# Performance work log

Measured on AMD Instinct MI355X. Metric: run time of the kernel, lower is better.

## Reference

```python
import jax, jax.numpy as jnp
import numpy as np

NEG_INF = -9e15  # matches the -9000000000000000.0 mask constant in the torch code
ALPHA = 0.2      # LeakyReLU negative slope


def setup_inputs() -> dict:
    key = jax.random.key(0)
    ks = jax.random.split(key, 8)
    N, F = 8192, 256
    h = jax.random.normal(ks[0], (N, F), dtype=jnp.float32)
    adj = jax.random.randint(ks[1], (N, N), 0, 2).astype(jnp.float32)
    W = jax.random.normal(ks[2], (F, F), dtype=jnp.float32) * 0.05
    a = jax.random.normal(ks[3], (2 * F, 1), dtype=jnp.float32) * 0.05
    w_ih = jax.random.normal(ks[4], (3 * F, F), dtype=jnp.float32) * 0.05
    w_hh = jax.random.normal(ks[5], (3 * F, F), dtype=jnp.float32) * 0.05
    b_ih = jax.random.normal(ks[6], (3 * F,), dtype=jnp.float32) * 0.05
    b_hh = jax.random.normal(ks[7], (3 * F,), dtype=jnp.float32) * 0.05
    return {"h": h, "adj": adj, "W": W, "a": a,
            "w_ih": w_ih, "w_hh": w_hh, "b_ih": b_ih, "b_hh": b_hh}


def reference(h, adj, W, a, w_ih, w_hh, b_ih, b_hh):
    F_out = W.shape[1]
    Wh = h @ W  # [N, F]
    # a_input @ a decomposes exactly: e_ij = leakyrelu(Wh_i . a[:F] + Wh_j . a[F:])
    src = Wh @ a[:F_out]   # [N, 1]
    dst = Wh @ a[F_out:]   # [N, 1]
    e = jax.nn.leaky_relu(src + dst.T, ALPHA)          # [N, N]
    att = jnp.where(adj > 0, e, NEG_INF)
    att = jax.nn.softmax(att, axis=1)                   # dropout: eval mode (identity)
    h_prime = att @ Wh                                  # [N, F]
    # torch GRUCell(h_prime, h)
    gi = h_prime @ w_ih.T + b_ih                        # [N, 3F]
    gh = h @ w_hh.T + b_hh
    i_r, i_z, i_n = jnp.split(gi, 3, axis=1)
    h_r, h_z, h_n = jnp.split(gh, 3, axis=1)
    r = jax.nn.sigmoid(i_r + h_r)
    z = jax.nn.sigmoid(i_z + h_z)
    n = jnp.tanh(i_n + r * h_n)
    return (1.0 - z) * n + z * h
```

## Files before the change

kernel.cpp:

```cpp
#include <hip/hip_runtime.h>

typedef __attribute__((ext_vector_type(8))) short bf16x8;
typedef __attribute__((ext_vector_type(4))) float f32x4;
typedef unsigned short u16;

#define NN 8192
#define FD 256

__device__ __forceinline__ u16 f2bf(float f) {
  union { float f; unsigned u; } v; v.f = f;
  unsigned r = v.u + 0x7FFF + ((v.u >> 16) & 1);
  return (u16)(r >> 16);
}

__device__ __forceinline__ bf16x8 ldcvt8(const float* __restrict__ p) {
  f32x4 x0 = *(const f32x4*)p;
  f32x4 x1 = *(const f32x4*)(p + 4);
  bf16x8 t;
  t[0] = (short)f2bf(x0[0]); t[1] = (short)f2bf(x0[1]);
  t[2] = (short)f2bf(x0[2]); t[3] = (short)f2bf(x0[3]);
  t[4] = (short)f2bf(x1[0]); t[5] = (short)f2bf(x1[1]);
  t[6] = (short)f2bf(x1[2]); t[7] = (short)f2bf(x1[3]);
  return t;
}

__global__ __launch_bounds__(256) void k_zero(float* __restrict__ p) {
  size_t g = (size_t)(blockIdx.x * 256 + threadIdx.x) * 4;
  f32x4 z = {0.f, 0.f, 0.f, 0.f};
  *(f32x4*)(p + g) = z;
}

__global__ __launch_bounds__(256) void k_wh(const float* __restrict__ h,
                                            const float* __restrict__ W,
                                            const float* __restrict__ a,
                                            u16* __restrict__ whT,
                                            float* __restrict__ src,
                                            float* __restrict__ dst) {
  int tid = threadIdx.x;
  int lane = tid & 63;
  int wv = tid >> 6;
  int r0 = blockIdx.x * 64 + (wv >> 1) * 32;
  int c0 = blockIdx.y * 64 + (wv & 1) * 32;
  int lr = lane & 15;
  int q = lane >> 4;

  f32x4 acc[2][2] = {};
  for (int kk = 0; kk < FD; kk += 32) {
    int kb = kk + q * 8;
    bf16x8 av[2], bv[2];
#pragma unroll
    for (int m = 0; m < 2; m++)
      av[m] = ldcvt8(h + (size_t)(r0 + m * 16 + lr) * FD + kb);
#pragma unroll
    for (int n = 0; n < 2; n++) {
      int col = c0 + n * 16 + lr;
      const float* p = W + (size_t)kb * FD + col;
      bf16x8 t;
#pragma unroll
      for (int e = 0; e < 8; e++) t[e] = (short)f2bf(p[(size_t)e * FD]);
      bv[n] = t;
    }
#pragma unroll
    for (int m = 0; m < 2; m++)
#pragma unroll
      for (int n = 0; n < 2; n++)
        acc[m][n] = __builtin_amdgcn_mfma_f32_16x16x32_bf16(av[m], bv[n], acc[m][n], 0, 0, 0);
  }
#pragma unroll
  for (int m = 0; m < 2; m++)
#pragma unroll
    for (int n = 0; n < 2; n++) {
      int gc = c0 + n * 16 + lr;
      int gr = r0 + m * 16 + q * 4;
      ushort4 st;
      st.x = f2bf(acc[m][n][0]);
      st.y = f2bf(acc[m][n][1]);
      st.z = f2bf(acc[m][n][2]);
      st.w = f2bf(acc[m][n][3]);
      *(ushort4*)(whT + (size_t)gc * NN + gr) = st;
    }
  float aA0 = a[c0 + lr], aA1 = a[c0 + 16 + lr];
  float aB0 = a[256 + c0 + lr], aB1 = a[256 + c0 + 16 + lr];
#pragma unroll
  for (int m = 0; m < 2; m++)
#pragma unroll
    for (int j = 0; j < 4; j++) {
      float s1 = acc[m][0][j] * aA0 + acc[m][1][j] * aA1;
      float s2 = acc[m][0][j] * aB0 + acc[m][1][j] * aB1;
#pragma unroll
      for (int sh = 1; sh < 16; sh <<= 1) {
        s1 += __shfl_xor(s1, sh);
        s2 += __shfl_xor(s2, sh);
      }
      if (lr == 0) {
        int row = r0 + m * 16 + q * 4 + j;
        atomicAdd(&src[row], s1);
        atomicAdd(&dst[row], s2);
      }
    }
}

__global__ __launch_bounds__(512, 4) void k_att(const float* __restrict__ adj,
                                                const u16* __restrict__ whT,
                                                const float* __restrict__ src,
                                                const float* __restrict__ dst,
                                                float* __restrict__ hp,
                                                float* __restrict__ lg) {
  __shared__ u16 pbuf[3][4096];
  __shared__ float dst_lds[2048];
  __shared__ float lred[8][64];

  const int tid = threadIdx.x;
  const int lane = tid & 63;
  const int w = tid >> 6;
  const int lr = lane & 15;
  const int q = lane >> 4;
  const int bid = blockIdx.x;
  const int jh = bid & 3;
  const int i0 = (bid >> 2) * 64;
  const int jb = jh * 2048;

  const int pi = lane;
  const float* adjP = adj + (size_t)(i0 + pi) * NN + jb + w * 8;
  const float srcv = src[i0 + pi];
  const int c0 = w * 32;
  const u16* wp = whT + (size_t)(c0 + lr) * NN + jb + q * 8;
  const int pw = (pi * 64 + w * 8) ^ ((pi & 7) << 3);

  f32x4 ar0[2], ar1[2];
  bf16x8 B0[2][2], B1[2][2];
  f32x4 acc[4][2] = {};
  float lsum = 0.f;

  *(f32x4*)&dst_lds[tid * 4] = *(const f32x4*)(dst + jb + tid * 4);

#define AL(S, AR)                                                              \
  { AR[0] = *(const f32x4*)(adjP + (size_t)(S) * 64);                          \
    AR[1] = *(const f32x4*)(adjP + (size_t)(S) * 64 + 4); }
#define BL(S, B)                                                               \
  { _Pragma("unroll") for (int kh = 0; kh < 2; kh++)                           \
    _Pragma("unroll") for (int n = 0; n < 2; n++)                              \
      B[kh][n] = *(const bf16x8*)(wp + (size_t)n * 16 * NN + (S) * 64 + kh * 32); }
#define PS(S, AR, WB)                                                          \
  {                                                                            \
    bf16x8 s0;                                                                 \
    _Pragma("unroll") for (int v = 0; v < 2; v++)                              \
      _Pragma("unroll") for (int e = 0; e < 4; e++) {                          \
        float x = srcv + dst_lds[(S) * 64 + w * 8 + v * 4 + e];                \
        x = fmaxf(x, 0.2f * x);                                                \
        float p = AR[v][e] * __expf(x);                                        \
        lsum += p;                                                             \
        s0[v * 4 + e] = (short)f2bf(p);                                        \
      }                                                                        \
    *(bf16x8*)&pbuf[WB][pw] = s0;                                              \
  }
#define CMPS(RB, B)                                                            \
  {                                                                            \
    _Pragma("unroll") for (int m = 0; m < 4; m++)                              \
      _Pragma("unroll") for (int kh = 0; kh < 2; kh++) {                       \
        bf16x8 pf = *(const bf16x8*)&pbuf[RB][((m * 16 + lr) * 64 + kh * 32 + q * 8) ^ ((lr & 7) << 3)]; \
        acc[m][0] = __builtin_amdgcn_mfma_f32_16x16x32_bf16(pf, B[kh][0], acc[m][0], 0, 0, 0); \
        acc[m][1] = __builtin_amdgcn_mfma_f32_16x16x32_bf16(pf, B[kh][1], acc[m][1], 0, 0, 0); \
      }                                                                        \
  }
#define LBAR asm volatile("s_waitcnt lgkmcnt(0)\n\ts_barrier" ::: "memory")

  AL(0, ar0);
  AL(1, ar1);
  BL(0, B0);
  __syncthreads();
  PS(0, ar0, 0);
  LBAR;

  int rb = 0, wb = 1;
  for (int t = 0; t < 32; t += 2) {
    if (t + 2 < 32) AL(t + 2, ar0);
    PS(t + 1, ar1, wb);
    BL(t + 1, B1);
    CMPS(rb, B0);
    LBAR;
    rb = wb; wb = (wb == 2) ? 0 : wb + 1;
    if (t + 3 < 32) AL(t + 3, ar1);
    if (t + 2 < 32) {
      PS(t + 2, ar0, wb);
      BL(t + 2, B0);
    }
    CMPS(rb, B1);
    LBAR;
    rb = wb; wb = (wb == 2) ? 0 : wb + 1;
  }
#undef AL
#undef BL
#undef PS
#undef CMPS
#undef LBAR

  lred[w][pi] = lsum;
  __syncthreads();
  if (tid < 64) {
    float l = 0.f;
#pragma unroll
    for (int v = 0; v < 8; v++) l += lred[v][tid];
    atomicAdd(&lg[i0 + tid], l);
  }
#pragma unroll
  for (int m = 0; m < 4; m++)
#pragma unroll
    for (int n = 0; n < 2; n++)
#pragma unroll
      for (int j = 0; j < 4; j++)
        atomicAdd(&hp[(size_t)(i0 + m * 16 + q * 4 + j) * FD + c0 + n * 16 + lr],
                  acc[m][n][j]);
}

__global__ __launch_bounds__(256) void k_norm(const float* __restrict__ hp,
                                              const float* __restrict__ lg,
                                              u16* __restrict__ hpb) {
  int g = blockIdx.x * 1024 + threadIdx.x * 4;
  f32x4 v = *(const f32x4*)(hp + g);
  float inv = 1.0f / lg[g >> 8];
  ushort4 st;
  st.x = f2bf(v[0] * inv);
  st.y = f2bf(v[1] * inv);
  st.z = f2bf(v[2] * inv);
  st.w = f2bf(v[3] * inv);
  *(ushort4*)(hpb + g) = st;
}

__global__ __launch_bounds__(256) void k_gru(const u16* __restrict__ hpb,
                                             const float* __restrict__ h,
                                             const float* __restrict__ wih,
                                             const float* __restrict__ whh,
                                             const float* __restrict__ bih,
                                             const float* __restrict__ bhh,
                                             float* __restrict__ out) {
  int tid = threadIdx.x;
  int lane = tid & 63;
  int wv = tid >> 6;
  int i0 = blockIdx.x * 32;
  int lr = lane & 15;
  int q = lane >> 4;
  int c = blockIdx.y * 64 + wv * 16 + lr;
  f32x4 gi[3][2] = {};
  f32x4 gh[3][2] = {};
  for (int kk = 0; kk < FD; kk += 32) {
    int kb = kk + q * 8;
    bf16x8 ap[2], ah[2], bi[3], bh[3];
#pragma unroll
    for (int m = 0; m < 2; m++) {
      ap[m] = *(const bf16x8*)(hpb + (size_t)(i0 + m * 16 + lr) * FD + kb);
      ah[m] = ldcvt8(h + (size_t)(i0 + m * 16 + lr) * FD + kb);
    }
#pragma unroll
    for (int g = 0; g < 3; g++) {
      bi[g] = ldcvt8(wih + (size_t)(g * 256 + c) * FD + kb);
      bh[g] = ldcvt8(whh + (size_t)(g * 256 + c) * FD + kb);
    }
#pragma unroll
    for (int g = 0; g < 3; g++)
#pragma unroll
      for (int m = 0; m < 2; m++) {
        gi[g][m] = __builtin_amdgcn_mfma_f32_16x16x32_bf16(ap[m], bi[g], gi[g][m], 0, 0, 0);
        gh[g][m] = __builtin_amdgcn_mfma_f32_16x16x32_bf16(ah[m], bh[g], gh[g][m], 0, 0, 0);
      }
  }
  float bir = bih[c], biz = bih[256 + c], bin = bih[512 + c];
  float bhr = bhh[c], bhz = bhh[256 + c], bhn = bhh[512 + c];
#pragma unroll
  for (int m = 0; m < 2; m++)
#pragma unroll
    for (int j = 0; j < 4; j++) {
      int row = i0 + m * 16 + q * 4 + j;
      float rv = gi[0][m][j] + bir + gh[0][m][j] + bhr;
      float zv = gi[1][m][j] + biz + gh[1][m][j] + bhz;
      float r = 1.f / (1.f + __expf(-rv));
      float z = 1.f / (1.f + __expf(-zv));
      float nx = gi[2][m][j] + bin + r * (gh[2][m][j] + bhn);
      float n = 1.f - 2.f / (__expf(2.f * nx) + 1.f);
      float hv = h[(size_t)row * FD + c];
      out[(size_t)row * FD + c] = (1.f - z) * n + z * hv;
    }
}

extern "C" void kernel_launch(void* const* d_in, const int* in_sizes, int n_in,
                              void* d_out, int out_size, void* d_ws, size_t ws_size,
                              hipStream_t stream) {
  const float* h   = (const float*)d_in[0];
  const float* adj = (const float*)d_in[1];
  const float* W   = (const float*)d_in[2];
  const float* a   = (const float*)d_in[3];
  const float* wih = (const float*)d_in[4];
  const float* whh = (const float*)d_in[5];
  const float* bih = (const float*)d_in[6];
  const float* bhh = (const float*)d_in[7];
  float* out = (float*)d_out;

  char* ws = (char*)d_ws;
  u16* whT   = (u16*)(ws);
  u16* hpb   = (u16*)(ws);
  float* hp  = (float*)(ws + 4194304);
  float* lg  = (float*)(ws + 12582912);
  float* srcv = (float*)(ws + 12615680);
  float* dstv = (float*)(ws + 12648448);
  (void)ws_size;

  k_zero<<<2072, 256, 0, stream>>>((float*)(ws + 4194304));
  k_wh<<<dim3(128, 4), 256, 0, stream>>>(h, W, a, whT, srcv, dstv);
  k_att<<<512, 512, 0, stream>>>(adj, whT, srcv, dstv, hp, lg);
  k_norm<<<2048, 256, 0, stream>>>(hp, lg, hpb);
  k_gru<<<dim3(256, 4), 256, 0, stream>>>(hpb, h, wih, whh, bih, bhh, out);
}
```

Before: 215.9 us.

## Restructure attention kernel to stage Wh tiles in LDS via direct global-to-LDS loads

The attention-aggregation kernel is reorganised so each wave owns a 16-row by 128-column output tile. Probabilities are computed directly in registers as the MFMA A operand, which drops the shared probability buffer. The Wh^T tiles are streamed into a 4-stage LDS ring with global_load_lds and read back with a swizzled pattern, and a vmcnt-aware barrier allows loads to overlap compute. The aim is to cut the LDS write/read round-trip for probabilities and the redundant per-wave global loads of Wh. The trade-offs are duplicated exp work (two column-half waves recompute the same probabilities) and larger LDS use, which may lower occupancy.

```diff
diff --git a/kernel.cpp b/kernel.cpp
--- a/kernel.cpp
+++ b/kernel.cpp
@@ -3,6 +3,7 @@
 typedef __attribute__((ext_vector_type(8))) short bf16x8;
 typedef __attribute__((ext_vector_type(4))) float f32x4;
 typedef unsigned short u16;
+typedef unsigned int u32;
 
 #define NN 8192
 #define FD 256
@@ -22,6 +23,11 @@
   t[4] = (short)f2bf(x1[0]); t[5] = (short)f2bf(x1[1]);
   t[6] = (short)f2bf(x1[2]); t[7] = (short)f2bf(x1[3]);
   return t;
+}
+
+__device__ __forceinline__ void gl16(const void* g, void* l) {
+  __builtin_amdgcn_global_load_lds((const __attribute__((address_space(1))) u32*)g,
+                                   (__attribute__((address_space(3))) u32*)l, 16, 0, 0);
 }
 
 __global__ __launch_bounds__(256) void k_zero(float* __restrict__ p) {
@@ -106,111 +112,110 @@
                                                 const float* __restrict__ dst,
                                                 float* __restrict__ hp,
                                                 float* __restrict__ lg) {
-  __shared__ u16 pbuf[3][4096];
+  __shared__ u16 wbuf[4][8192];
   __shared__ float dst_lds[2048];
-  __shared__ float lred[8][64];
 
   const int tid = threadIdx.x;
   const int lane = tid & 63;
   const int w = tid >> 6;
   const int lr = lane & 15;
   const int q = lane >> 4;
+  const int rg = w >> 1;
+  const int ch = w & 1;
   const int bid = blockIdx.x;
   const int jh = bid & 3;
   const int i0 = (bid >> 2) * 64;
   const int jb = jh * 2048;
 
-  const int pi = lane;
-  const float* adjP = adj + (size_t)(i0 + pi) * NN + jb + w * 8;
-  const float srcv = src[i0 + pi];
-  const int c0 = w * 32;
-  const u16* wp = whT + (size_t)(c0 + lr) * NN + jb + q * 8;
-  const int pw = (pi * 64 + w * 8) ^ ((pi & 7) << 3);
-
-  f32x4 ar0[2], ar1[2];
-  bf16x8 B0[2][2], B1[2][2];
-  f32x4 acc[4][2] = {};
+  const float* adjP = adj + (size_t)(i0 + rg * 16 + lr) * NN + jb + q * 8;
+  const float srcv = src[i0 + rg * 16 + lr];
+
+  const int gc = w * 32 + (lane >> 2);
+  const int jslot = (lane & 3) ^ ((lane >> 3) & 3);
+  const u16* wsrc0 = whT + (size_t)gc * NN + jb + jslot * 8;
+  const u16* wsrc1 = wsrc0 + (size_t)16 * NN;
+
+  const int dsb = (ch * 128 + lr) * 32 + (q ^ ((lr >> 1) & 3)) * 8;
+
+  f32x4 acc[8] = {};
   float lsum = 0.f;
+  f32x4 aA0, aA1, aB0, aB1;
+  bf16x8 AF;
+
+#define G(T)                                                                \
+  {                                                                         \
+    gl16(wsrc0 + (size_t)(T) * 32, &wbuf[(T) & 3][w * 1024]);               \
+    gl16(wsrc1 + (size_t)(T) * 32, &wbuf[(T) & 3][w * 1024 + 512]);         \
+  }
+#define ALOAD(T, R0, R1)                                                    \
+  {                                                                         \
+    R0 = *(const f32x4*)(adjP + (size_t)(T) * 32);                          \
+    R1 = *(const f32x4*)(adjP + (size_t)(T) * 32 + 4);                      \
+  }
+#define ACOMP(T, R0, R1)                                                    \
+  {                                                                         \
+    f32x4 d0 = *(const f32x4*)&dst_lds[(T) * 32 + q * 8];                   \
+    f32x4 d1 = *(const f32x4*)&dst_lds[(T) * 32 + q * 8 + 4];               \
+    _Pragma("unroll") for (int e = 0; e < 4; e++) {                         \
+      float x = srcv + d0[e];                                               \
+      x = fmaxf(x, 0.2f * x);                                               \
+      float p = R0[e] * __expf(x);                                          \
+      lsum += p;                                                            \
+      AF[e] = (short)f2bf(p);                                               \
+    }                                                                       \
+    _Pragma("unroll") for (int e = 0; e < 4; e++) {                         \
+      float x = srcv + d1[e];                                               \
+      x = fmaxf(x, 0.2f * x);                                               \
+      float p = R1[e] * __expf(x);                                          \
+      lsum += p;                                                            \
+      AF[4 + e] = (short)f2bf(p);                                           \
+    }                                                                       \
+  }
+#define CMPS(T)                                                             \
+  {                                                                         \
+    const u16* pb = &wbuf[(T) & 3][0];                                      \
+    _Pragma("unroll") for (int bn = 0; bn < 8; bn++) {                      \
+      bf16x8 bf = *(const bf16x8*)&pb[dsb + bn * 512];                      \
+      acc[bn] = __builtin_amdgcn_mfma_f32_16x16x32_bf16(AF, bf, acc[bn], 0, 0, 0); \
+    }                                                                       \
+  }
+#define LBARV asm volatile("s_waitcnt vmcnt(6) lgkmcnt(0)\n\ts_barrier" ::: "memory")
 
   *(f32x4*)&dst_lds[tid * 4] = *(const f32x4*)(dst + jb + tid * 4);
-
-#define AL(S, AR)                                                              \
-  { AR[0] = *(const f32x4*)(adjP + (size_t)(S) * 64);                          \
-    AR[1] = *(const f32x4*)(adjP + (size_t)(S) * 64 + 4); }
-#define BL(S, B)                                                               \
-  { _Pragma("unroll") for (int kh = 0; kh < 2; kh++)                           \
-    _Pragma("unroll") for (int n = 0; n < 2; n++)                              \
-      B[kh][n] = *(const bf16x8*)(wp + (size_t)n * 16 * NN + (S) * 64 + kh * 32); }
-#define PS(S, AR, WB)                                                          \
-  {                                                                            \
-    bf16x8 s0;                                                                 \
-    _Pragma("unroll") for (int v = 0; v < 2; v++)                              \
-      _Pragma("unroll") for (int e = 0; e < 4; e++) {                          \
-        float x = srcv + dst_lds[(S) * 64 + w * 8 + v * 4 + e];                \
-        x = fmaxf(x, 0.2f * x);                                                \
-        float p = AR[v][e] * __expf(x);                                        \
-        lsum += p;                                                             \
-        s0[v * 4 + e] = (short)f2bf(p);                                        \
-      }                                                                        \
-    *(bf16x8*)&pbuf[WB][pw] = s0;                                              \
-  }
-#define CMPS(RB, B)                                                            \
-  {                                                                            \
-    _Pragma("unroll") for (int m = 0; m < 4; m++)                              \
-      _Pragma("unroll") for (int kh = 0; kh < 2; kh++) {                       \
-        bf16x8 pf = *(const bf16x8*)&pbuf[RB][((m * 16 + lr) * 64 + kh * 32 + q * 8) ^ ((lr & 7) << 3)]; \
-        acc[m][0] = __builtin_amdgcn_mfma_f32_16x16x32_bf16(pf, B[kh][0], acc[m][0], 0, 0, 0); \
-        acc[m][1] = __builtin_amdgcn_mfma_f32_16x16x32_bf16(pf, B[kh][1], acc[m][1], 0, 0, 0); \
-      }                                                                        \
-  }
-#define LBAR asm volatile("s_waitcnt lgkmcnt(0)\n\ts_barrier" ::: "memory")
-
-  AL(0, ar0);
-  AL(1, ar1);
-  BL(0, B0);
+  G(0);
+  G(1);
+  ALOAD(0, aA0, aA1);
+  ALOAD(1, aB0, aB1);
   __syncthreads();
-  PS(0, ar0, 0);
-  LBAR;
-
-  int rb = 0, wb = 1;
-  for (int t = 0; t < 32; t += 2) {
-    if (t + 2 < 32) AL(t + 2, ar0);
-    PS(t + 1, ar1, wb);
-    BL(t + 1, B1);
-    CMPS(rb, B0);
-    LBAR;
-    rb = wb; wb = (wb == 2) ? 0 : wb + 1;
-    if (t + 3 < 32) AL(t + 3, ar1);
-    if (t + 2 < 32) {
-      PS(t + 2, ar0, wb);
-      BL(t + 2, B0);
-    }
-    CMPS(rb, B1);
-    LBAR;
-    rb = wb; wb = (wb == 2) ? 0 : wb + 1;
-  }
-#undef AL
-#undef BL
-#undef PS
+
+  for (int t = 0; t < 64; t += 2) {
+    if (t + 2 < 64) G(t + 2);
+    ACOMP(t, aA0, aA1);
+    if (t + 2 < 64) ALOAD(t + 2, aA0, aA1);
+    LBARV;
+    CMPS(t);
+    if (t + 3 < 64) G(t + 3);
+    ACOMP(t + 1, aB0, aB1);
+    if (t + 3 < 64) ALOAD(t + 3, aB0, aB1);
+    LBARV;
+    CMPS(t + 1);
+  }
+#undef G
+#undef ALOAD
+#undef ACOMP
 #undef CMPS
-#undef LBAR
-
-  lred[w][pi] = lsum;
-  __syncthreads();
-  if (tid < 64) {
-    float l = 0.f;
-#pragma unroll
-    for (int v = 0; v < 8; v++) l += lred[v][tid];
-    atomicAdd(&lg[i0 + tid], l);
-  }
-#pragma unroll
-  for (int m = 0; m < 4; m++)
-#pragma unroll
-    for (int n = 0; n < 2; n++)
-#pragma unroll
-      for (int j = 0; j < 4; j++)
-        atomicAdd(&hp[(size_t)(i0 + m * 16 + q * 4 + j) * FD + c0 + n * 16 + lr],
-                  acc[m][n][j]);
+#undef LBARV
+
+  lsum += __shfl_xor(lsum, 16);
+  lsum += __shfl_xor(lsum, 32);
+  if (ch == 0 && q == 0) atomicAdd(&lg[i0 + rg * 16 + lr], lsum);
+
+#pragma unroll
+  for (int bn = 0; bn < 8; bn++)
+#pragma unroll
+    for (int j = 0; j < 4; j++)
+      atomicAdd(&hp[(size_t)(i0 + rg * 16 + q * 4 + j) * FD + ch * 128 + bn * 16 + lr],
+                acc[bn][j]);
 }
 
 __global__ __launch_bounds__(256) void k_norm(const float* __restrict__ hp,
```

Result: slower. 229.9 us (+6.5%).
